# Kernel tuning notes

Measured on AMD Instinct MI355X. Metric: run time of the kernel, lower is better.

Reference implementation:

```python
import jax, jax.numpy as jnp
import numpy as np

HEADS = 8
DIM_HEAD = 64
IMG = 32            # image_size
K = 5               # kernel_size
DIL = 1             # dilation
SEQ_LEN = 1279
SCALE = DIM_HEAD ** -0.5
IMG_SEQ = IMG * IMG                 # 1024
TEXT_LEN = SEQ_LEN + 1 - IMG_SEQ    # 256
NEG = -np.finfo(np.float32).max


def _unfold(img, pad_value):
    """torch F.unfold equivalent. img: [B, C, H, W] -> [B, H*W, K*K, C].
    Kernel-position index j is fastest-varying (matches torch unfold ordering
    after rearrange 'b (d j) i -> b i j d')."""
    B, C, H, W = img.shape
    p = ((K - 1) * DIL + 1) // 2
    padded = jnp.pad(img, ((0, 0), (0, 0), (p, p), (p, p)), constant_values=pad_value)
    patches = [padded[:, :, i * DIL:i * DIL + H, j * DIL:j * DIL + W]
               for i in range(K) for j in range(K)]
    pt = jnp.stack(patches, axis=2)            # [B, C, K*K, H, W]
    return pt.reshape(B, C, K * K, H * W).transpose(0, 3, 2, 1)


def _split_heads(t, b):
    # [b, N, h*d] -> [(b h), N, d]  (b slow, h fast)
    N = t.shape[1]
    return t.reshape(b, N, HEADS, DIM_HEAD).transpose(0, 2, 1, 3).reshape(b * HEADS, N, DIM_HEAD)


def setup_inputs() -> dict:
    key = jax.random.key(0)
    k1, k2, k3, k4 = jax.random.split(key, 4)
    dim = 512
    inner = HEADS * DIM_HEAD
    x = jax.random.normal(k1, (4, 1279, dim), dtype=jnp.float32)
    mask = jnp.ones((4, TEXT_LEN), dtype=bool)
    W_qkv = jax.random.normal(k2, (dim, inner * 3), dtype=jnp.float32) * 0.02
    W_out = jax.random.normal(k3, (inner, dim), dtype=jnp.float32) * 0.02
    b_out = jax.random.normal(k4, (dim,), dtype=jnp.float32) * 0.02
    return {"x": x, "mask": mask, "W_qkv": W_qkv, "W_out": W_out, "b_out": b_out}


def reference(x, mask, W_qkv, W_out, b_out):
    b, n, dim = x.shape
    pad = SEQ_LEN - n + 1
    xp = jnp.pad(x, ((0, 0), (0, pad), (0, 0)))            # [b, SEQ_LEN+1, dim]
    mask = mask[:, :TEXT_LEN]

    qkv = xp @ W_qkv
    q, k, v = jnp.split(qkv, 3, axis=-1)
    q = _split_heads(q, b) * SCALE                          # [(bh), N, d]
    k = _split_heads(k, b)
    v = _split_heads(v, b)

    q_text, q_img = q[:, :-IMG_SEQ], q[:, -IMG_SEQ:]
    k_text, k_img = k[:, :-IMG_SEQ], k[:, -IMG_SEQ:]
    v_text, v_img = v[:, :-IMG_SEQ], v[:, -IMG_SEQ:]

    # ---- text-to-text causal attention ----
    dots_text = jnp.einsum('bid,bjd->bij', q_text, k_text)
    tl = TEXT_LEN
    text_causal = jnp.triu(jnp.ones((tl, tl), dtype=bool), 1)
    dots_text = jnp.where(text_causal[None], NEG, dots_text)
    attn_text = jax.nn.softmax(dots_text, axis=-1)
    out_text = jnp.einsum('bij,bjd->bid', attn_text, v_text)

    # ---- local-window image attention (unfold) ----
    bh = b * HEADS
    k_img2 = k_img.reshape(bh, IMG, IMG, DIM_HEAD).transpose(0, 3, 1, 2)
    v_img2 = v_img.reshape(bh, IMG, IMG, DIM_HEAD).transpose(0, 3, 1, 2)
    k_imgu = _unfold(k_img2, 0.0)                           # [(bh), IMG_SEQ, K*K, d]
    v_imgu = _unfold(v_img2, 0.0)

    dots_image = jnp.einsum('bid,bijd->bij', q_img, k_imgu)         # [(bh), IMG_SEQ, K*K]
    dots_i2t = jnp.einsum('bid,bjd->bij', q_img, k_text)            # [(bh), IMG_SEQ, tl]

    # causal mask over local window via unfolded position indices
    idx = jnp.arange(IMG_SEQ, dtype=jnp.float32).reshape(1, 1, IMG, IMG)
    k_idx = _unfold(idx, float(IMG_SEQ))[..., 0]            # [1, IMG_SEQ, K*K]
    q_idx = jnp.arange(IMG_SEQ, dtype=jnp.float32)[None, :, None]
    causal_mask = q_idx < k_idx                             # [1, IMG_SEQ, K*K]

    text_pad_mask = jnp.repeat(~mask, HEADS, axis=0)[:, None, :]    # [(bh), 1, tl]
    full_mask = jnp.concatenate([
        jnp.broadcast_to(text_pad_mask, (bh, IMG_SEQ, tl)),
        jnp.broadcast_to(causal_mask, (bh, IMG_SEQ, K * K)),
    ], axis=-1)

    dots = jnp.concatenate([dots_i2t, dots_image], axis=-1)
    dots = jnp.where(full_mask, NEG, dots)
    attn = jax.nn.softmax(dots, axis=-1)
    attn_i2t, attn_img = attn[..., :tl], attn[..., tl:]

    out_image = (jnp.einsum('bij,bijd->bid', attn_img, v_imgu)
                 + jnp.einsum('bij,bjd->bid', attn_i2t, v_text))

    # ---- merge and project ----
    out = jnp.concatenate([out_text, out_image], axis=1)    # [(bh), N, d]
    N = out.shape[1]
    out = out.reshape(b, HEADS, N, DIM_HEAD).transpose(0, 2, 1, 3).reshape(b, N, HEADS * DIM_HEAD)
    out = out @ W_out + b_out
    return out[:, :n]
```

## Files before the change

### kernel.cpp

```cpp
#include <hip/hip_runtime.h>
#include <hip/hip_bf16.h>
#include <math.h>

#define HEADS   8
#define DH      64
#define IMGW    32
#define KKER    5
#define SEQ     1280
#define NTOK    1279
#define TL      256
#define IMG_SEQ 1024
#define DIM     512
#define BATCH   4
#define BH      32
#define SCALE   0.125f
#define NEGB    (-1.0e30f)

#define WQN  (DIM * 3 * DIM)
#define WON  (DIM * DIM)
#define QKVN ((size_t)BH * SEQ * DH)
#define AON  ((size_t)BATCH * SEQ * DIM)

#define XPBLK   1280
#define WQTILES 768
#define WOTILES 256


typedef unsigned short u16;
typedef __attribute__((ext_vector_type(8))) short bf16x8;
typedef __attribute__((ext_vector_type(4))) float f32x4;

__device__ inline u16 f2b(float f) {
    unsigned int u = __float_as_uint(f);
    return (u16)((u + 0x7FFFu + ((u >> 16) & 1u)) >> 16);
}
__device__ inline unsigned pack2(float a, float b) {
    return (unsigned)f2b(a) | ((unsigned)f2b(b) << 16);
}

__device__ inline void ldsload16(const u16* g, u16* l) {
    __builtin_amdgcn_global_load_lds(
        (const __attribute__((address_space(1))) unsigned int*)g,
        (__attribute__((address_space(3))) unsigned int*)l, 16, 0, 0);
}

__device__ inline void lds_barrier() {
    asm volatile("s_waitcnt lgkmcnt(0)\n\ts_barrier" ::: "memory");
}

__global__ __launch_bounds__(256) void cvt_all(
    const float* __restrict__ x, const float* __restrict__ Wq,
    const float* __restrict__ Wo, u16* __restrict__ xbf,
    u16* __restrict__ WqT, u16* __restrict__ WoT)
{
    __shared__ u16 tile[32][33];
    const int b = blockIdx.x;
    if (b < XPBLK) {
        const int i = b * 256 + threadIdx.x;
        const int row = i >> 6;
        const int bb = row / SEQ, nn = row % SEQ;
        union { unsigned u[4]; bf16x8 v; } r;
        if (nn < NTOK) {
            const size_t j = ((size_t)(bb * NTOK + nn) * 128 + (i & 63) * 2);
            const float4 a = ((const float4*)x)[j];
            const float4 c = ((const float4*)x)[j + 1];
            r.u[0] = pack2(a.x, a.y); r.u[1] = pack2(a.z, a.w);
            r.u[2] = pack2(c.x, c.y); r.u[3] = pack2(c.z, c.w);
        } else {
            r.u[0] = r.u[1] = r.u[2] = r.u[3] = 0u;
        }
        ((bf16x8*)xbf)[i] = r.v;
        return;
    }
    int t = b - XPBLK;
    const float* src; u16* dst; int C;
    if (t < WQTILES) { src = Wq; dst = WqT; C = 3 * DIM; }
    else             { t -= WQTILES; src = Wo; dst = WoT; C = DIM; }
    const int tc = C / 32;
    const int tr0 = (t / tc) * 32, tc0 = (t % tc) * 32;
    const int ty = threadIdx.x >> 5, tx = threadIdx.x & 31;
    #pragma unroll
    for (int s = 0; s < 4; s++) {
        const int r = ty + 8 * s;
        tile[r][tx] = f2b(src[(size_t)(tr0 + r) * C + tc0 + tx]);
    }
    __syncthreads();
    #pragma unroll
    for (int s = 0; s < 4; s++) {
        const int c = ty + 8 * s;
        dst[(size_t)(tc0 + c) * DIM + tr0 + tx] = tile[tx][c];
    }
}

__global__ __launch_bounds__(256) void qkv_mfma6(
    const u16* __restrict__ xbf, const u16* __restrict__ WqT,
    u16* __restrict__ Qbf, u16* __restrict__ Kbf, u16* __restrict__ VTbf)
{
    __shared__ u16 pool[12288];
    u16* const buf0 = pool;
    u16* const buf1 = pool + 6144;
    const int tid  = threadIdx.x;
    const int lane = tid & 63, wave = tid >> 6;
    const int quad = lane >> 4, l16 = lane & 15;
    const int wm = (wave >> 1) * 32, wn = (wave & 1) * 64;
    const int m0 = blockIdx.y * 64, n0 = blockIdx.x * 128;

    const u16* ga  = xbf + (size_t)(m0 + (tid >> 2)) * DIM + (tid & 3) * 8;
    const u16* gb0 = WqT + (size_t)(n0 + (tid >> 2)) * DIM + (tid & 3) * 8;
    const u16* gb1 = WqT + (size_t)(n0 + 64 + (tid >> 2)) * DIM + (tid & 3) * 8;

    f32x4 acc[2][4];
    #pragma unroll
    for (int i = 0; i < 2; i++)
        #pragma unroll
        for (int j = 0; j < 4; j++) acc[i][j] = (f32x4){0.f, 0.f, 0.f, 0.f};

    auto stage = [&](u16* b, int k) {
        ldsload16(ga  + k, b + wave * 512);
        ldsload16(gb0 + k, b + 2048 + wave * 512);
        ldsload16(gb1 + k, b + 4096 + wave * 512);
    };
    auto comp = [&](const u16* b) {
        bf16x8 af_[2], bf_[4];
        #pragma unroll
        for (int i = 0; i < 2; i++)
            af_[i] = *(const bf16x8*)&b[(wm + i * 16 + l16) * 32 + quad * 8];
        #pragma unroll
        for (int j = 0; j < 4; j++)
            bf_[j] = *(const bf16x8*)&b[2048 + (wn + j * 16 + l16) * 32 + quad * 8];
        #pragma unroll
        for (int i = 0; i < 2; i++)
            #pragma unroll
            for (int j = 0; j < 4; j++)
                acc[i][j] = __builtin_amdgcn_mfma_f32_16x16x32_bf16(
                    af_[i], bf_[j], acc[i][j], 0, 0, 0);
    };

    stage(buf0, 0);
    __syncthreads();
    for (int k0 = 0; k0 < DIM; k0 += 64) {
        stage(buf1, k0 + 32);
        comp(buf0);
        __syncthreads();
        if (k0 + 64 < DIM) stage(buf0, k0 + 64);
        comp(buf1);
        __syncthreads();
    }

    const int which = n0 >> 9;
    const float scl = (which == 0) ? SCALE : 1.f;
    #pragma unroll
    for (int i = 0; i < 2; i++)
        #pragma unroll
        for (int r = 0; r < 4; r++)
            #pragma unroll
            for (int j = 0; j < 4; j++)
                pool[(wm + i * 16 + quad * 4 + r) * 144 + wn + j * 16 + l16] =
                    f2b(acc[i][j][r] * scl);
    __syncthreads();

    const int b_  = m0 / SEQ;
    const int nn0 = m0 % SEQ;
    if (which < 2) {
        u16* base = (which == 0) ? Qbf : Kbf;
        #pragma unroll
        for (int s = 0; s < 4; s++) {
            const int c   = tid + 256 * s;
            const int row = c >> 4, c8 = (c & 15) * 8;
            const int col511 = (n0 + c8) & 511;
            const int h = col511 >> 6, d0 = col511 & 63;
            const int bhh = b_ * HEADS + h;
            const bf16x8 v = *(const bf16x8*)&pool[row * 144 + c8];
            *(bf16x8*)&base[((size_t)bhh * SEQ + nn0 + row) * DH + d0] = v;
        }
    } else {
        #pragma unroll
        for (int s = 0; s < 4; s++) {
            const int c   = tid + 256 * s;
            const int col = c & 127, r8 = (c >> 7) * 8;
            const int col511 = (n0 + col) & 511;
            const int h = col511 >> 6, d = col511 & 63;
            const int bhh = b_ * HEADS + h;
            union { u16 u[8]; bf16x8 v; } w;
            #pragma unroll
            for (int k = 0; k < 8; k++)
                w.u[k] = pool[(r8 + k) * 144 + col];
            *(bf16x8*)&VTbf[((size_t)bhh * DH + d) * SEQ + nn0 + r8] = w.v;
        }
    }
}

__global__ __launch_bounds__(256, 4) void attn_fused(
    const u16* __restrict__ Qbf, const u16* __restrict__ Kbf,
    const u16* __restrict__ VTbf, u16* __restrict__ AObf)
{
    const int id = blockIdx.x;
    const int bh = (id & 7) | (((id >> 3) & 3) << 3);
    const int bx = id >> 5;
    const bool istext = bx < 8;
    const int r0 = bx - 8;
    const int qt0 = istext ? bx * 32 : r0 * 32;
    const int qrow0 = istext ? qt0 : TL + qt0;
    const int tid = threadIdx.x;
    const int lane = tid & 63, wave = tid >> 6;
    const int quad = lane >> 4, l16 = lane & 15;

    __shared__ u16   Pb[32][424];
    __shared__ float wmaxs[4][32];
    __shared__ float wsums[4][32];

    const int krs = istext ? 0 : min(max(r0 - 2, 0), IMGW - 5);
    const int cbase = TL + krs * 32;
    const int nct = istext ? 0 : ((wave < 2) ? 3 : 2);
    const bool tactive = !istext || (2 * wave <= bx);

    bf16x8 af[2][2];
    #pragma unroll
    for (int i = 0; i < 2; i++) {
        const u16* qr = Qbf + ((size_t)bh * SEQ + qrow0 + i * 16 + l16) * DH;
        af[i][0] = *(const bf16x8*)(qr + quad * 8);
        af[i][1] = *(const bf16x8*)(qr + 32 + quad * 8);
    }

    const u16* kb = Kbf + (size_t)bh * SEQ * DH;

    f32x4 sacc[2][4], cacc[2][3];
    #pragma unroll
    for (int i = 0; i < 2; i++) {
        #pragma unroll
        for (int j = 0; j < 4; j++) sacc[i][j] = (f32x4){0.f, 0.f, 0.f, 0.f};
        #pragma unroll
        for (int s = 0; s < 3; s++) cacc[i][s] = (f32x4){0.f, 0.f, 0.f, 0.f};
    }

    if (tactive) {
        bf16x8 kf0[4], kf1[4];
        #pragma unroll
        for (int j = 0; j < 4; j++) {
            const int key = wave * 64 + j * 16 + l16;
            const u16* kp = kb + (size_t)key * DH + quad * 8;
            kf0[j] = *(const bf16x8*)(kp);
            kf1[j] = *(const bf16x8*)(kp + 32);
        }
        #pragma unroll
        for (int j = 0; j < 4; j++)
            #pragma unroll
            for (int i = 0; i < 2; i++) {
                sacc[i][j] = __builtin_amdgcn_mfma_f32_16x16x32_bf16(af[i][0], kf0[j], sacc[i][j], 0, 0, 0);
                sacc[i][j] = __builtin_amdgcn_mfma_f32_16x16x32_bf16(af[i][1], kf1[j], sacc[i][j], 0, 0, 0);
            }
    }
    if (!istext) {
        bf16x8 cf0[3], cf1[3];
        #pragma unroll
        for (int s = 0; s < 3; s++) {
            if (s < nct) {
                const int t = wave + 4 * s;
                const u16* kp = kb + (size_t)(cbase + t * 16 + l16) * DH + quad * 8;
                cf0[s] = *(const bf16x8*)(kp);
                cf1[s] = *(const bf16x8*)(kp + 32);
            }
        }
        #pragma unroll
        for (int s = 0; s < 3; s++) {
            if (s < nct) {
                #pragma unroll
                for (int i = 0; i < 2; i++) {
                    cacc[i][s] = __builtin_amdgcn_mfma_f32_16x16x32_bf16(af[i][0], cf0[s], cacc[i][s], 0, 0, 0);
                    cacc[i][s] = __builtin_amdgcn_mfma_f32_16x16x32_bf16(af[i][1], cf1[s], cacc[i][s], 0, 0, 0);
                }
            }
        }
    }

    const int mt = wave >> 1, nh = wave & 1;
    const u16* vtb = VTbf + (size_t)bh * DH * SEQ;
    const u16* vr0 = vtb + (size_t)(nh * 32 + l16) * SEQ + quad * 8;
    const u16* vr1 = vtb + (size_t)(nh * 32 + 16 + l16) * SEQ + quad * 8;
    bf16x8 v0[4], v1[4];
    #pragma unroll
    for (int p = 0; p < 4; p++) {
        v0[p] = *(const bf16x8*)(vr0 + p * 32);
        v1[p] = *(const bf16x8*)(vr1 + p * 32);
    }

    float m8[2][4];
    #pragma unroll
    for (int i = 0; i < 2; i++)
        #pragma unroll
        for (int r = 0; r < 4; r++) {
            const int q = i * 16 + quad * 4 + r;
            float m = NEGB;
            if (istext) {
                if (tactive) {
                    const int qg = qt0 + q;
                    #pragma unroll
                    for (int j = 0; j < 4; j++) {
                        const int key = wave * 64 + j * 16 + l16;
                        const float v = (key <= qg) ? sacc[i][j][r] : NEGB;
                        sacc[i][j][r] = v;
                        m = fmaxf(m, v);
                    }
                }
            } else {
                const int qi = qt0 + q;
                #pragma unroll
                for (int j = 0; j < 4; j++) m = fmaxf(m, sacc[i][j][r]);
                #pragma unroll
                for (int s = 0; s < 3; s++) {
                    if (s < nct) {
                        const int t = wave + 4 * s;
                        const int kidx = krs * 32 + t * 16 + l16;
                        const int kr = kidx >> 5, kc = kidx & 31;
                        const bool valid = (abs(kr - r0) <= 2) && (abs(kc - q) <= 2)
                                           && (kidx <= qi);
                        const float v = valid ? cacc[i][s][r] : NEGB;
                        cacc[i][s][r] = v;
                        m = fmaxf(m, v);
                    }
                }
            }
            m8[i][r] = m;
        }
    #pragma unroll
    for (int off = 1; off < 16; off <<= 1)
        #pragma unroll
        for (int i = 0; i < 2; i++)
            #pragma unroll
            for (int r = 0; r < 4; r++)
                m8[i][r] = fmaxf(m8[i][r], __shfl_xor(m8[i][r], off));
    if (l16 == 0)
        #pragma unroll
        for (int i = 0; i < 2; i++)
            #pragma unroll
            for (int r = 0; r < 4; r++)
                wmaxs[wave][i * 16 + quad * 4 + r] = m8[i][r];
    lds_barrier();

    float s8[2][4];
    #pragma unroll
    for (int i = 0; i < 2; i++)
        #pragma unroll
        for (int r = 0; r < 4; r++) {
            const int q = i * 16 + quad * 4 + r;
            const float mr = fmaxf(fmaxf(wmaxs[0][q], wmaxs[1][q]),
                                   fmaxf(wmaxs[2][q], wmaxs[3][q]));
            float s = 0.f;
            if (tactive) {
                #pragma unroll
                for (int j = 0; j < 4; j++) {
                    const float p = __expf(sacc[i][j][r] - mr);
                    Pb[q][wave * 64 + j * 16 + l16] = f2b(p);
                    s += p;
                }
            }
            #pragma unroll
            for (int ss = 0; ss < 3; ss++) {
                if (ss < nct) {
                    const int t = wave + 4 * ss;
                    const float p = __expf(cacc[i][ss][r] - mr);
                    Pb[q][256 + t * 16 + l16] = f2b(p);
                    s += p;
                }
            }
            s8[i][r] = s;
        }
    #pragma unroll
    for (int off = 1; off < 16; off <<= 1)
        #pragma unroll
        for (int i = 0; i < 2; i++)
            #pragma unroll
            for (int r = 0; r < 4; r++)
                s8[i][r] += __shfl_xor(s8[i][r], off);
    if (l16 == 0)
        #pragma unroll
        for (int i = 0; i < 2; i++)
            #pragma unroll
            for (int r = 0; r < 4; r++)
                wsums[wave][i * 16 + quad * 4 + r] = s8[i][r];
    lds_barrier();

    f32x4 oacc[2];
    oacc[0] = (f32x4){0.f, 0.f, 0.f, 0.f};
    oacc[1] = (f32x4){0.f, 0.f, 0.f, 0.f};
    const int nch = istext ? (bx + 1) : 13;
    #pragma unroll
    for (int ch = 0; ch < 13; ch++) {
        if (ch < nch) {
            const bf16x8 a = *(const bf16x8*)&Pb[mt * 16 + l16][ch * 32 + quad * 8];
            const bf16x8 c0 = v0[ch & 3], c1 = v1[ch & 3];
            const int chn = ch + 4;
            if (chn < nch) {
                const int kc = (chn < 8) ? chn * 32 : (cbase + (chn - 8) * 32);
                v0[ch & 3] = *(const bf16x8*)(vr0 + kc);
                v1[ch & 3] = *(const bf16x8*)(vr1 + kc);
            }
            oacc[0] = __builtin_amdgcn_mfma_f32_16x16x32_bf16(a, c0, oacc[0], 0, 0, 0);
            oacc[1] = __builtin_amdgcn_mfma_f32_16x16x32_bf16(a, c1, oacc[1], 0, 0, 0);
        }
    }
    const int b_ = bh >> 3, h = bh & 7;
    #pragma unroll
    for (int r = 0; r < 4; r++) {
        const int q = mt * 16 + quad * 4 + r;
        const float si = 1.f / ((wsums[0][q] + wsums[1][q]) + (wsums[2][q] + wsums[3][q]));
        u16* dst = AObf + ((size_t)b_ * SEQ + qrow0 + q) * DIM + h * DH + nh * 32;
        dst[l16]      = f2b(oacc[0][r] * si);
        dst[l16 + 16] = f2b(oacc[1][r] * si);
    }
}

__global__ __launch_bounds__(256) void proj_mfma6(
    const u16* __restrict__ AObf, const u16* __restrict__ WoT,
    const float* __restrict__ bias, float* __restrict__ out)
{
    __shared__ u16 pool[10240];
    u16* const buf0 = pool;
    u16* const buf1 = pool + 5120;
    const int tid  = threadIdx.x;
    const int lane = tid & 63, wave = tid >> 6;
    const int quad = lane >> 4, l16 = lane & 15;
    const int wm = (wave >> 1) * 16, wn = (wave & 1) * 64;
    const int m0 = blockIdx.y * 32, n0 = blockIdx.x * 128;

    const u16* ga  = AObf + (size_t)(m0 + ((tid & 127) >> 2)) * DIM + (tid & 3) * 8;
    const u16* gb0 = WoT + (size_t)(n0 + (tid >> 2)) * DIM + (tid & 3) * 8;
    const u16* gb1 = WoT + (size_t)(n0 + 64 + (tid >> 2)) * DIM + (tid & 3) * 8;

    f32x4 acc[4];
    #pragma unroll
    for (int j = 0; j < 4; j++) acc[j] = (f32x4){0.f, 0.f, 0.f, 0.f};

    auto stage = [&](u16* b, int k) {
        if (wave < 2) ldsload16(ga + k, b + (wave & 1) * 512);
        ldsload16(gb0 + k, b + 1024 + wave * 512);
        ldsload16(gb1 + k, b + 3072 + wave * 512);
    };
    auto comp = [&](const u16* b) {
        const bf16x8 af = *(const bf16x8*)&b[(wm + l16) * 32 + quad * 8];
        bf16x8 bf_[4];
        #pragma unroll
        for (int j = 0; j < 4; j++)
            bf_[j] = *(const bf16x8*)&b[1024 + (wn + j * 16 + l16) * 32 + quad * 8];
        #pragma unroll
        for (int j = 0; j < 4; j++)
            acc[j] = __builtin_amdgcn_mfma_f32_16x16x32_bf16(af, bf_[j], acc[j], 0, 0, 0);
    };

    stage(buf0, 0);
    __syncthreads();
    for (int k0 = 0; k0 < DIM; k0 += 64) {
        stage(buf1, k0 + 32);
        comp(buf0);
        __syncthreads();
        if (k0 + 64 < DIM) stage(buf0, k0 + 64);
        comp(buf1);
        __syncthreads();
    }

    #pragma unroll
    for (int r = 0; r < 4; r++) {
        const int mm = m0 + wm + quad * 4 + r;
        const int bb = mm / SEQ, nn = mm % SEQ;
        if (nn >= NTOK) continue;
        const size_t mr = (size_t)(bb * NTOK + nn);
        #pragma unroll
        for (int j = 0; j < 4; j++) {
            const int ncol = n0 + wn + j * 16 + l16;
            out[mr * DIM + ncol] = acc[j][r] + bias[ncol];
        }
    }
}

extern "C" void kernel_launch(void* const* d_in, const int* in_sizes, int n_in,
                              void* d_out, int out_size, void* d_ws, size_t ws_size,
                              hipStream_t stream)
{
    const float* x    = (const float*)d_in[0];
    const float* Wqkv = (const float*)d_in[2];
    const float* Wout = (const float*)d_in[3];
    const float* bout = (const float*)d_in[4];
    float* out = (float*)d_out;

    u16* wsu  = (u16*)d_ws;
    u16* xbf  = wsu;
    u16* WqT  = xbf + AON;
    u16* WoT  = WqT + WQN;
    u16* Qbf  = WoT + WON;
    u16* Kbf  = Qbf + QKVN;
    u16* VTbf = Kbf + QKVN;
    u16* AObf = VTbf + QKVN;

    cvt_all   <<<XPBLK + WQTILES + WOTILES, 256, 0, stream>>>(x, Wqkv, Wout, xbf, WqT, WoT);
    qkv_mfma6 <<<dim3(12, 80), 256, 0, stream>>>(xbf, WqT, Qbf, Kbf, VTbf);
    attn_fused<<<dim3(40 * BH), 256, 0, stream>>>(Qbf, Kbf, VTbf, AObf);
    proj_mfma6<<<dim3(4, 160), 256, 0, stream>>>(AObf, WoT, bout, out);
}
```

Baseline: 126.4 us.

## Split softmax per wave with local max and merge partial outputs

Each wave now runs the softmax on its own key slice with a wave-local max. It writes P into a private LDS region and computes a partial P·V over its own keys for all 64 output dims, so one block barrier is removed and the P matrix is no longer shared across waves. The partial outputs and per-wave max and sum statistics are then merged in LDS with rescaling weights, and each thread writes one vectorized bf16x8 of the output. In exchange, V is loaded per wave with no prefetch pipeline, each wave does more MFMAs on fewer keys, and the larger fp32 LDS footprint may reduce occupancy.

```diff
diff --git a/kernel.cpp b/kernel.cpp
--- a/kernel.cpp
+++ b/kernel.cpp
@@ -205,14 +205,16 @@
     const int lane = tid & 63, wave = tid >> 6;
     const int quad = lane >> 4, l16 = lane & 15;
 
-    __shared__ u16   Pb[32][424];
-    __shared__ float wmaxs[4][32];
-    __shared__ float wsums[4][32];
+    __shared__ float Opool[4][2176];
+    __shared__ float msm[4][32];
+    __shared__ float mss[4][32];
 
     const int krs = istext ? 0 : min(max(r0 - 2, 0), IMGW - 5);
     const int cbase = TL + krs * 32;
     const int nct = istext ? 0 : ((wave < 2) ? 3 : 2);
     const bool tactive = !istext || (2 * wave <= bx);
+
+    u16* const Pw = (u16*)Opool[wave];
 
     bf16x8 af[2][2];
     #pragma unroll
@@ -271,17 +273,6 @@
                 }
             }
         }
-    }
-
-    const int mt = wave >> 1, nh = wave & 1;
-    const u16* vtb = VTbf + (size_t)bh * DH * SEQ;
-    const u16* vr0 = vtb + (size_t)(nh * 32 + l16) * SEQ + quad * 8;
-    const u16* vr1 = vtb + (size_t)(nh * 32 + 16 + l16) * SEQ + quad * 8;
-    bf16x8 v0[4], v1[4];
-    #pragma unroll
-    for (int p = 0; p < 4; p++) {
-        v0[p] = *(const bf16x8*)(vr0 + p * 32);
-        v1[p] = *(const bf16x8*)(vr1 + p * 32);
     }
 
     float m8[2][4];
@@ -329,13 +320,6 @@
             #pragma unroll
             for (int r = 0; r < 4; r++)
                 m8[i][r] = fmaxf(m8[i][r], __shfl_xor(m8[i][r], off));
-    if (l16 == 0)
-        #pragma unroll
-        for (int i = 0; i < 2; i++)
-            #pragma unroll
-            for (int r = 0; r < 4; r++)
-                wmaxs[wave][i * 16 + quad * 4 + r] = m8[i][r];
-    lds_barrier();
 
     float s8[2][4];
     #pragma unroll
@@ -343,26 +327,26 @@
         #pragma unroll
         for (int r = 0; r < 4; r++) {
             const int q = i * 16 + quad * 4 + r;
-            const float mr = fmaxf(fmaxf(wmaxs[0][q], wmaxs[1][q]),
-                                   fmaxf(wmaxs[2][q], wmaxs[3][q]));
+            const float mr = m8[i][r];
             float s = 0.f;
             if (tactive) {
                 #pragma unroll
                 for (int j = 0; j < 4; j++) {
                     const float p = __expf(sacc[i][j][r] - mr);
-                    Pb[q][wave * 64 + j * 16 + l16] = f2b(p);
+                    Pw[q * 136 + j * 16 + l16] = f2b(p);
                     s += p;
                 }
             }
             #pragma unroll
             for (int ss = 0; ss < 3; ss++) {
                 if (ss < nct) {
-                    const int t = wave + 4 * ss;
                     const float p = __expf(cacc[i][ss][r] - mr);
-                    Pb[q][256 + t * 16 + l16] = f2b(p);
+                    Pw[q * 136 + 64 + ss * 16 + l16] = f2b(p);
                     s += p;
                 }
             }
+            if (!istext && wave < 2)
+                Pw[q * 136 + 112 + l16] = 0;
             s8[i][r] = s;
         }
     #pragma unroll
@@ -376,38 +360,88 @@
         #pragma unroll
         for (int i = 0; i < 2; i++)
             #pragma unroll
+            for (int r = 0; r < 4; r++) {
+                const int q = i * 16 + quad * 4 + r;
+                msm[wave][q] = m8[i][r];
+                mss[wave][q] = s8[i][r];
+            }
+    asm volatile("s_waitcnt lgkmcnt(0)" ::: "memory");
+
+    bool cact[4];
+    int ka[4], kbb[4];
+    ka[0] = wave * 64;      kbb[0] = ka[0] + 16;
+    ka[1] = wave * 64 + 32; kbb[1] = ka[1] + 16;
+    if (istext) {
+        cact[0] = tactive; cact[1] = (2 * wave + 1 <= bx);
+        cact[2] = false;   cact[3] = false;
+        ka[2] = kbb[2] = ka[3] = kbb[3] = 0;
+    } else {
+        cact[0] = cact[1] = cact[2] = true; cact[3] = (wave < 2);
+        ka[2] = cbase + wave * 16;       kbb[2] = cbase + (wave + 4) * 16;
+        ka[3] = cbase + (wave + 8) * 16; kbb[3] = ka[3];
+    }
+
+    const u16* vtb = VTbf + (size_t)bh * DH * SEQ;
+    f32x4 o2[2][4];
+    #pragma unroll
+    for (int i = 0; i < 2; i++)
+        #pragma unroll
+        for (int j = 0; j < 4; j++) o2[i][j] = (f32x4){0.f, 0.f, 0.f, 0.f};
+
+    #pragma unroll
+    for (int c = 0; c < 4; c++) {
+        if (cact[c]) {
+            const int key = (quad < 2) ? (ka[c] + quad * 8)
+                                       : (kbb[c] + (quad - 2) * 8);
+            const bf16x8 av0 = *(const bf16x8*)&Pw[l16 * 136 + c * 32 + quad * 8];
+            const bf16x8 av1 = *(const bf16x8*)&Pw[(16 + l16) * 136 + c * 32 + quad * 8];
+            bf16x8 bv[4];
+            #pragma unroll
+            for (int j = 0; j < 4; j++)
+                bv[j] = *(const bf16x8*)(vtb + (size_t)(j * 16 + l16) * SEQ + key);
+            #pragma unroll
+            for (int j = 0; j < 4; j++) {
+                o2[0][j] = __builtin_amdgcn_mfma_f32_16x16x32_bf16(av0, bv[j], o2[0][j], 0, 0, 0);
+                o2[1][j] = __builtin_amdgcn_mfma_f32_16x16x32_bf16(av1, bv[j], o2[1][j], 0, 0, 0);
+            }
+        }
+    }
+
+    #pragma unroll
+    for (int i = 0; i < 2; i++)
+        #pragma unroll
+        for (int j = 0; j < 4; j++)
+            #pragma unroll
             for (int r = 0; r < 4; r++)
-                wsums[wave][i * 16 + quad * 4 + r] = s8[i][r];
+                Opool[wave][(i * 16 + quad * 4 + r) * 68 + j * 16 + l16] = o2[i][j][r];
+
     lds_barrier();
 
-    f32x4 oacc[2];
-    oacc[0] = (f32x4){0.f, 0.f, 0.f, 0.f};
-    oacc[1] = (f32x4){0.f, 0.f, 0.f, 0.f};
-    const int nch = istext ? (bx + 1) : 13;
-    #pragma unroll
-    for (int ch = 0; ch < 13; ch++) {
-        if (ch < nch) {
-            const bf16x8 a = *(const bf16x8*)&Pb[mt * 16 + l16][ch * 32 + quad * 8];
-            const bf16x8 c0 = v0[ch & 3], c1 = v1[ch & 3];
-            const int chn = ch + 4;
-            if (chn < nch) {
-                const int kc = (chn < 8) ? chn * 32 : (cbase + (chn - 8) * 32);
-                v0[ch & 3] = *(const bf16x8*)(vr0 + kc);
-                v1[ch & 3] = *(const bf16x8*)(vr1 + kc);
-            }
-            oacc[0] = __builtin_amdgcn_mfma_f32_16x16x32_bf16(a, c0, oacc[0], 0, 0, 0);
-            oacc[1] = __builtin_amdgcn_mfma_f32_16x16x32_bf16(a, c1, oacc[1], 0, 0, 0);
-        }
-    }
+    const int qq = tid >> 3, d8 = (tid & 7) * 8;
+    const float mm = fmaxf(fmaxf(msm[0][qq], msm[1][qq]),
+                           fmaxf(msm[2][qq], msm[3][qq]));
+    float wgt[4];
+    float den = 0.f;
+    #pragma unroll
+    for (int w = 0; w < 4; w++) {
+        wgt[w] = __expf(msm[w][qq] - mm);
+        den += mss[w][qq] * wgt[w];
+    }
+    float o[8];
+    #pragma unroll
+    for (int e = 0; e < 8; e++) o[e] = 0.f;
+    #pragma unroll
+    for (int w = 0; w < 4; w++) {
+        const float* Ow = &Opool[w][qq * 68 + d8];
+        #pragma unroll
+        for (int e = 0; e < 8; e++) o[e] += Ow[e] * wgt[w];
+    }
+    const float inv = 1.f / den;
+    union { u16 u[8]; bf16x8 v; } pk;
+    #pragma unroll
+    for (int e = 0; e < 8; e++) pk.u[e] = f2b(o[e] * inv);
     const int b_ = bh >> 3, h = bh & 7;
-    #pragma unroll
-    for (int r = 0; r < 4; r++) {
-        const int q = mt * 16 + quad * 4 + r;
-        const float si = 1.f / ((wsums[0][q] + wsums[1][q]) + (wsums[2][q] + wsums[3][q]));
-        u16* dst = AObf + ((size_t)b_ * SEQ + qrow0 + q) * DIM + h * DH + nh * 32;
-        dst[l16]      = f2b(oacc[0][r] * si);
-        dst[l16 + 16] = f2b(oacc[1][r] * si);
-    }
+    *(bf16x8*)&AObf[((size_t)b_ * SEQ + qrow0 + qq) * DIM + h * DH + d8] = pk.v;
 }
 
 __global__ __launch_bounds__(256) void proj_mfma6(
```

New measurement: 121.6 us. -3.8%, faster.
